# Performance work log

Measured on AMD Instinct MI355X. Metric: run time of the kernel, lower is better.

The kernel has to match this reference:

```python
import jax, jax.numpy as jnp
import numpy as np

B, S, HID = 2, 2048, 2048
H, KV, D = 16, 8, 128          # heads, kv heads, head_dim
GROUPS = H // KV               # 2
RATIO = 0.5
SCALING = D ** -0.5
MIN = float(np.finfo(np.float32).min)


def rotate_half(x):
    x1, x2 = x[..., : D // 2], x[..., D // 2 :]
    return jnp.concatenate((-x2, x1), axis=-1)


def setup_inputs() -> dict:
    key = jax.random.key(0)
    ks = jax.random.split(key, 9)
    hidden_states = jax.random.normal(ks[0], (B, S, HID), jnp.float32)
    # rotary tables (bounded like real cos/sin)
    cos = jax.random.uniform(ks[1], (B, S, D), jnp.float32)
    sin = jax.random.uniform(ks[2], (B, S, D), jnp.float32)
    # additive causal mask [B,1,S,S]: 0 where allowed, finfo.min above diagonal
    causal = jnp.triu(jnp.ones((S, S), bool), k=1)
    attention_mask = jnp.where(causal, MIN, 0.0).astype(jnp.float32)[None, None]
    attention_mask = jnp.broadcast_to(attention_mask, (B, 1, S, S))
    sd = 1.0 / np.sqrt(HID)
    Wq = jax.random.normal(ks[3], (H * D, HID), jnp.float32) * sd
    Wk = jax.random.normal(ks[4], (KV * D, HID), jnp.float32) * sd
    Wv = jax.random.normal(ks[5], (KV * D, HID), jnp.float32) * sd
    A = jax.random.normal(ks[6], (H,), jnp.float32) * 0.1
    Wdt = jax.random.normal(ks[7], (H, KV * D), jnp.float32) * (1.0 / np.sqrt(KV * D))
    Wo = jax.random.normal(ks[8], (HID, H * D), jnp.float32) * (1.0 / np.sqrt(H * D))
    return {"hidden_states": hidden_states, "cos": cos, "sin": sin,
            "attention_mask": attention_mask, "Wq": Wq, "Wk": Wk, "Wv": Wv,
            "A": A, "Wdt": Wdt, "Wo": Wo}


def reference(hidden_states, cos, sin, attention_mask, Wq, Wk, Wv, A, Wdt, Wo):
    x = hidden_states
    # fused QKV projections -> [B, heads, S, D]
    q = (x @ Wq.T).reshape(B, S, H, D).transpose(0, 2, 1, 3)
    k = (x @ Wk.T).reshape(B, S, KV, D).transpose(0, 2, 1, 3)
    v = (x @ Wv.T).reshape(B, S, KV, D).transpose(0, 2, 1, 3)
    # RoPE (cos/sin unsqueezed on head dim)
    c, s = cos[:, None], sin[:, None]
    q = q * c + rotate_half(q) * s
    k = k * c + rotate_half(k) * s
    # dynamic mask: dt_proj(value) -> softplus -> exp, per head  [B, H, S]
    v_flat = v.transpose(0, 2, 1, 3).reshape(B, S, KV * D)
    dt = v_flat @ Wdt.T                                    # [B,S,H]
    dyn = jnp.exp(A * jax.nn.softplus(dt)).transpose(0, 2, 1)  # [B,H,S]
    # kthvalue thresholding (k-th smallest along keys)
    num_dyn = int(S * RATIO)                               # 1024
    kth = jnp.sort(dyn, axis=-1)[..., num_dyn - 1 : num_dyn]   # [B,H,1]
    attn_mask = jnp.where(dyn < kth, MIN, dyn)[:, :, None, :]  # [B,H,1,S]
    attn_mask = attn_mask + attention_mask                 # [B,H,S,S]
    # GQA repeat kv
    k_rep = jnp.repeat(k, GROUPS, axis=1)
    v_rep = jnp.repeat(v, GROUPS, axis=1)
    scores = jnp.einsum("bhqd,bhkd->bhqk", q, k_rep) * SCALING + attn_mask
    w = jax.nn.softmax(scores.astype(jnp.float32), axis=-1).astype(q.dtype)
    out = jnp.einsum("bhqk,bhkd->bhqd", w, v_rep)
    out = out.transpose(0, 2, 1, 3).reshape(B, S, H * D)
    return out @ Wo.T
```

## Files before the change

### kernel.cpp

```cpp
#include <hip/hip_runtime.h>

typedef unsigned short u16;
typedef _Float16 f16x8 __attribute__((ext_vector_type(8)));
typedef float f32x4 __attribute__((ext_vector_type(4)));
typedef u16 u16x8 __attribute__((ext_vector_type(8)));

#define MINF (-0x1.fffffep+127f)
#define SCALE 0.08838834764831845f

__device__ __forceinline__ u16 f2h(float f) {
    _Float16 h = (_Float16)f;
    return __builtin_bit_cast(u16, h);
}
__device__ __forceinline__ float h2f(u16 u) {
    _Float16 h = __builtin_bit_cast(_Float16, u);
    return (float)h;
}

typedef const __attribute__((address_space(1))) void* gptr_t;
typedef __attribute__((address_space(3))) void* sptr_t;
#define GLDS16(g, l) __builtin_amdgcn_global_load_lds((gptr_t)(const void*)(g), (sptr_t)(void*)(l), 16, 0, 0)

__global__ void convk8(const float* __restrict__ in, u16* __restrict__ out, int n) {
    int i = (blockIdx.x * 256 + threadIdx.x) * 8;
    if (i >= n) return;
    f32x4 a = *(const f32x4*)&in[i];
    f32x4 b = *(const f32x4*)&in[i + 4];
    u16x8 r;
#pragma unroll
    for (int j = 0; j < 4; ++j) { r[j] = f2h(a[j]); r[j + 4] = f2h(b[j]); }
    *(u16x8*)&out[i] = r;
}

__global__ void convw3(const float* __restrict__ Wq, const float* __restrict__ Wk,
                       const float* __restrict__ Wv, u16* __restrict__ out) {
    int i = (blockIdx.x * 256 + threadIdx.x) * 8;
    const float* src;
    int off;
    if (i < 4194304) { src = Wq; off = i; }
    else if (i < 6291456) { src = Wk; off = i - 4194304; }
    else { src = Wv; off = i - 6291456; }
    f32x4 a = *(const f32x4*)&src[off];
    f32x4 b = *(const f32x4*)&src[off + 4];
    u16x8 r;
#pragma unroll
    for (int j = 0; j < 4; ++j) { r[j] = f2h(a[j]); r[j + 4] = f2h(b[j]); }
    *(u16x8*)&out[i] = r;
}

__global__ __launch_bounds__(512, 1) void gemm8_qkv(
    const u16* __restrict__ A, const u16* __restrict__ Bw,
    u16* __restrict__ qo, u16* __restrict__ ko, u16* __restrict__ vto) {
    __shared__ alignas(16) u16 AS[2][2][128 * 64];
    __shared__ alignas(16) u16 BS[2][2][128 * 64];
    const int K = 2048, NT = 32;
    int tid = threadIdx.x;
    int wid = tid >> 6, lane = tid & 63;
    int l16 = lane & 15, lhi = lane >> 4;
    int wm = wid >> 2, wn = wid & 3;
    int bm = blockIdx.y * 256, bn = blockIdx.x * 256;
    int srow = lane >> 3;
    int schunk = (lane & 7) ^ srow;
    f32x4 acc[8][4] = {};

    auto STAGE = [&](int t, int buf) {
        int kt = t * 64;
#pragma unroll
        for (int i = 0; i < 2; ++i) {
            int c = wid * 2 + i;
            int row = c * 8 + srow;
            const u16* sa0 = A + (size_t)(bm + row) * K + kt + schunk * 8;
            GLDS16(sa0, &AS[buf][0][c * 512]);
            const u16* sa1 = A + (size_t)(bm + 128 + row) * K + kt + schunk * 8;
            GLDS16(sa1, &AS[buf][1][c * 512]);
            const u16* sb0 = Bw + (size_t)(bn + row) * K + kt + schunk * 8;
            GLDS16(sb0, &BS[buf][0][c * 512]);
            const u16* sb1 = Bw + (size_t)(bn + 128 + row) * K + kt + schunk * 8;
            GLDS16(sb1, &BS[buf][1][c * 512]);
        }
    };

    auto COMPUTE = [&](int buf) {
#pragma unroll
        for (int kk = 0; kk < 2; ++kk) {
            f16x8 af[8], bf[4];
#pragma unroll
            for (int ni = 0; ni < 4; ++ni) {
                int rb = wn * 64 + ni * 16 + l16;
                int half = rb >> 7, rh = rb & 127;
                int c2 = (kk * 4 + lhi) ^ (rh & 7);
                bf[ni] = *(const f16x8*)&BS[buf][half][rh * 64 + c2 * 8];
            }
#pragma unroll
            for (int mi = 0; mi < 8; ++mi) {
                int rh = mi * 16 + l16;
                int c2 = (kk * 4 + lhi) ^ (rh & 7);
                af[mi] = *(const f16x8*)&AS[buf][wm][rh * 64 + c2 * 8];
            }
            __builtin_amdgcn_s_setprio(1);
#pragma unroll
            for (int mi = 0; mi < 8; ++mi)
#pragma unroll
                for (int ni = 0; ni < 4; ++ni)
                    acc[mi][ni] = __builtin_amdgcn_mfma_f32_16x16x32_f16(af[mi], bf[ni], acc[mi][ni], 0, 0, 0);
            __builtin_amdgcn_s_setprio(0);
        }
    };

    STAGE(0, 0);
    STAGE(1, 1);
    asm volatile("s_waitcnt vmcnt(8)" ::: "memory");
    __builtin_amdgcn_sched_barrier(0);
    __builtin_amdgcn_s_barrier();

    for (int t = 0; t < NT; ++t) {
        int buf = t & 1;
        COMPUTE(buf);
        __builtin_amdgcn_s_barrier();
        if (t + 2 < NT) {
            STAGE(t + 2, buf);
            asm volatile("s_waitcnt vmcnt(8)" ::: "memory");
        } else {
            asm volatile("s_waitcnt vmcnt(0)" ::: "memory");
        }
        __builtin_amdgcn_sched_barrier(0);
        __builtin_amdgcn_s_barrier();
    }

#pragma unroll
    for (int mi = 0; mi < 8; ++mi) {
#pragma unroll
        for (int ni = 0; ni < 4; ++ni) {
#pragma unroll
            for (int j = 0; j < 4; ++j) {
                int r = bm + wm * 128 + mi * 16 + lhi * 4 + j;
                int c = bn + wn * 64 + ni * 16 + l16;
                u16 hv = f2h(acc[mi][ni][j]);
                int b = r >> 11, s = r & 2047;
                if (c < 2048) {
                    int hh = c >> 7, d = c & 127;
                    qo[(((size_t)(b * 16 + hh)) * 2048 + s) * 128 + d] = hv;
                } else if (c < 3072) {
                    int hh = (c - 2048) >> 7, d = c & 127;
                    ko[(((size_t)(b * 8 + hh)) * 2048 + s) * 128 + d] = hv;
                } else {
                    int hh = (c - 3072) >> 7, d = c & 127;
                    vto[(((size_t)(b * 8 + hh)) * 128 + d) * 2048 + s] = hv;
                }
            }
        }
    }
}

__global__ __launch_bounds__(512, 1) void gemm8_op(
    const u16* __restrict__ A, const u16* __restrict__ Bw, float* __restrict__ Cf) {
    __shared__ alignas(16) u16 AS[2][2][128 * 64];
    __shared__ alignas(16) u16 BS[2][128 * 64];
    const int K = 2048, NT = 32;
    int tid = threadIdx.x;
    int wid = tid >> 6, lane = tid & 63;
    int l16 = lane & 15, lhi = lane >> 4;
    int wm = wid >> 2, wn = wid & 3;
    int bm = blockIdx.y * 256, bn = blockIdx.x * 128;
    int srow = lane >> 3;
    int schunk = (lane & 7) ^ srow;
    f32x4 acc[8][2] = {};

    auto STAGE = [&](int t, int buf) {
        int kt = t * 64;
#pragma unroll
        for (int i = 0; i < 2; ++i) {
            int c = wid * 2 + i;
            int row = c * 8 + srow;
            const u16* sa0 = A + (size_t)(bm + row) * K + kt + schunk * 8;
            GLDS16(sa0, &AS[buf][0][c * 512]);
            const u16* sa1 = A + (size_t)(bm + 128 + row) * K + kt + schunk * 8;
            GLDS16(sa1, &AS[buf][1][c * 512]);
            const u16* sb0 = Bw + (size_t)(bn + row) * K + kt + schunk * 8;
            GLDS16(sb0, &BS[buf][c * 512]);
        }
    };

    auto COMPUTE = [&](int buf) {
#pragma unroll
        for (int kk = 0; kk < 2; ++kk) {
            f16x8 af[8], bf[2];
#pragma unroll
            for (int ni = 0; ni < 2; ++ni) {
                int rb = wn * 32 + ni * 16 + l16;
                int c2 = (kk * 4 + lhi) ^ (rb & 7);
                bf[ni] = *(const f16x8*)&BS[buf][rb * 64 + c2 * 8];
            }
#pragma unroll
            for (int mi = 0; mi < 8; ++mi) {
                int rh = mi * 16 + l16;
                int c2 = (kk * 4 + lhi) ^ (rh & 7);
                af[mi] = *(const f16x8*)&AS[buf][wm][rh * 64 + c2 * 8];
            }
            __builtin_amdgcn_s_setprio(1);
#pragma unroll
            for (int mi = 0; mi < 8; ++mi)
#pragma unroll
                for (int ni = 0; ni < 2; ++ni)
                    acc[mi][ni] = __builtin_amdgcn_mfma_f32_16x16x32_f16(af[mi], bf[ni], acc[mi][ni], 0, 0, 0);
            __builtin_amdgcn_s_setprio(0);
        }
    };

    STAGE(0, 0);
    STAGE(1, 1);
    asm volatile("s_waitcnt vmcnt(6)" ::: "memory");
    __builtin_amdgcn_sched_barrier(0);
    __builtin_amdgcn_s_barrier();

    for (int t = 0; t < NT; ++t) {
        int buf = t & 1;
        COMPUTE(buf);
        __builtin_amdgcn_s_barrier();
        if (t + 2 < NT) {
            STAGE(t + 2, buf);
            asm volatile("s_waitcnt vmcnt(6)" ::: "memory");
        } else {
            asm volatile("s_waitcnt vmcnt(0)" ::: "memory");
        }
        __builtin_amdgcn_sched_barrier(0);
        __builtin_amdgcn_s_barrier();
    }

#pragma unroll
    for (int mi = 0; mi < 8; ++mi)
#pragma unroll
        for (int ni = 0; ni < 2; ++ni)
#pragma unroll
            for (int j = 0; j < 4; ++j) {
                int r = bm + wm * 128 + mi * 16 + lhi * 4 + j;
                int c = bn + wn * 32 + ni * 16 + l16;
                Cf[(size_t)r * 2048 + c] = acc[mi][ni][j];
            }
}

__global__ void rope_fused(u16* __restrict__ q, u16* __restrict__ k,
                           const float* __restrict__ cosv, const float* __restrict__ sinv) {
    int i = blockIdx.x * 256 + threadIdx.x;
    int d = i & 63;
    int s = (i >> 6) & 2047;
    int b = i >> 17;
    size_t cb = ((size_t)b * 2048 + s) * 128;
    float c1 = cosv[cb + d], s1 = sinv[cb + d];
    float c2 = cosv[cb + d + 64], s2 = sinv[cb + d + 64];
#pragma unroll
    for (int h = 0; h < 16; ++h) {
        size_t base = (((size_t)(b * 16 + h)) * 2048 + s) * 128;
        float x1 = h2f(q[base + d]), x2 = h2f(q[base + d + 64]);
        q[base + d] = f2h(x1 * c1 - x2 * s1);
        q[base + d + 64] = f2h(x2 * c2 + x1 * s2);
    }
#pragma unroll
    for (int h = 0; h < 8; ++h) {
        size_t base = (((size_t)(b * 8 + h)) * 2048 + s) * 128;
        float x1 = h2f(k[base + d]), x2 = h2f(k[base + d + 64]);
        k[base + d] = f2h(x1 * c1 - x2 * s1);
        k[base + d + 64] = f2h(x2 * c2 + x1 * s2);
    }
}

__global__ void wdtv_kernel(const float* __restrict__ Wdt, const float* __restrict__ Wv,
                            float* __restrict__ out) {
    int t = threadIdx.x;
    int h = blockIdx.x >> 3;
    int c = (blockIdx.x & 7) * 256 + t;
    const float* wd = Wdt + h * 1024;
    float acc = 0.f;
    for (int f = 0; f < 1024; ++f) acc += wd[f] * Wv[(size_t)f * 2048 + c];
    out[h * 2048 + c] = acc;
}

__global__ void dt_dyn_kernel(const float* __restrict__ x, const float* __restrict__ Wdtv,
                              const float* __restrict__ Av, float* __restrict__ dyn) {
    __shared__ float xrow[2048];
    __shared__ float red[256];
    int bs = blockIdx.x;
    int t = threadIdx.x;
    for (int i = t; i < 2048; i += 256) xrow[i] = x[(size_t)bs * 2048 + i];
    __syncthreads();
    int h = t & 15, chunk = t >> 4;
    float p = 0.f;
    const float* wrow = Wdtv + h * 2048 + chunk * 128;
    const float* xr = xrow + chunk * 128;
    for (int f = 0; f < 128; ++f) p += xr[f] * wrow[f];
    red[t] = p;
    __syncthreads();
    if (t < 16) {
        float dt = 0.f;
        for (int c = 0; c < 16; ++c) dt += red[c * 16 + t];
        float sp = fmaxf(dt, 0.f) + log1pf(expf(-fabsf(dt)));
        int b = bs >> 11, s = bs & 2047;
        dyn[((size_t)(b * 16 + t)) * 2048 + s] = expf(Av[t] * sp);
    }
}

__global__ void kth_mask_kernel(const float* __restrict__ dyn, float* __restrict__ mval) {
    __shared__ float sv[2048];
    int bh = blockIdx.x, t = threadIdx.x;
    const float* row = dyn + (size_t)bh * 2048;
    sv[t] = row[t];
    sv[t + 1024] = row[t + 1024];
    __syncthreads();
    for (int k = 2; k <= 2048; k <<= 1) {
        for (int j = k >> 1; j > 0; j >>= 1) {
#pragma unroll 1
            for (int base = 0; base < 2048; base += 1024) {
                int i = base + t;
                int ixj = i ^ j;
                if (ixj > i) {
                    float a = sv[i], b = sv[ixj];
                    bool up = ((i & k) == 0);
                    if ((a > b) == up) { sv[i] = b; sv[ixj] = a; }
                }
            }
            __syncthreads();
        }
    }
    float kth = sv[1023];
    float v0 = row[t];
    float v1 = row[t + 1024];
    mval[(size_t)bh * 2048 + t] = v0 < kth ? MINF : v0;
    mval[(size_t)bh * 2048 + t + 1024] = v1 < kth ? MINF : v1;
}

__global__ __launch_bounds__(256) void attn_kernel(
    const u16* __restrict__ qb, const u16* __restrict__ kb, const u16* __restrict__ vtb,
    const float* __restrict__ mv, u16* __restrict__ ao) {
    __shared__ alignas(16) u16 Kst[2][64 * 128];
    __shared__ alignas(16) u16 Vst[2][128 * 64];
    __shared__ alignas(16) u16 plds[4][16 * 72];
    __shared__ int flags[4];
    int bh = blockIdx.x;
    int qt = 31 - blockIdx.y;
    int b = bh >> 4, h = bh & 15, kvh = h >> 1;
    int wid = threadIdx.x >> 6, lane = threadIdx.x & 63;
    int l16 = lane & 15, lhi = lane >> 4;
    int q0 = qt * 64 + wid * 16;
    const u16* qbase = qb + (((size_t)bh * 2048) + q0) * 128;
    const u16* kbase = kb + ((size_t)(b * 8 + kvh) * 2048) * 128;
    const u16* vtbase = vtb + ((size_t)(b * 8 + kvh) * 128) * 2048;
    const float* mvb = mv + (size_t)bh * 2048;
    u16* pw = plds[wid];
    int rx = l16 & 7;

    auto STAGE = [&](int kt2, int bidx) {
        int kvb2 = kt2 * 64;
#pragma unroll
        for (int i = 0; i < 4; ++i) {
            int call = wid * 4 + i;
            int r = call * 4 + (lane >> 4);
            int gch = (lane & 15) ^ (r & 7);
            const u16* src = kbase + (size_t)(kvb2 + r) * 128 + gch * 8;
            GLDS16(src, &Kst[bidx][call * 512]);
        }
#pragma unroll
        for (int i = 0; i < 4; ++i) {
            int call = wid * 4 + i;
            int d = call * 8 + (lane >> 3);
            int gch = (lane & 7) ^ (d & 7);
            const u16* src = vtbase + (size_t)d * 2048 + kvb2 + gch * 8;
            GLDS16(src, &Vst[bidx][call * 512]);
        }
    };

    f16x8 qf[4];
#pragma unroll
    for (int kc = 0; kc < 4; ++kc) qf[kc] = *(const f16x8*)&qbase[l16 * 128 + kc * 32 + lhi * 8];
    f16x8 ones;
#pragma unroll
    for (int i = 0; i < 8; ++i) ones[i] = (_Float16)1.f;
    float m[4];
#pragma unroll
    for (int j = 0; j < 4; ++j) m[j] = -INFINITY;
    f32x4 accO[8] = {};
    f32x4 accS = {};

    STAGE(0, 0);
    __syncthreads();

    for (int kt = 0; kt < 32; ++kt) {
        if (kt > qt) {
            if (!(flags[0] | flags[1] | flags[2] | flags[3])) break;
        }
        int buf = kt & 1;
        if (kt + 1 < 32) STAGE(kt + 1, buf ^ 1);
        int kvb = kt * 64;

        f32x4 sc[4] = {};
#pragma unroll
        for (int ni = 0; ni < 4; ++ni) {
            const u16* kr = &Kst[buf][(ni * 16 + l16) * 128];
#pragma unroll
            for (int kc = 0; kc < 4; ++kc) {
                int cc = (kc * 4 + lhi) ^ rx;
                f16x8 kf = *(const f16x8*)&kr[cc * 8];
                sc[ni] = __builtin_amdgcn_mfma_f32_16x16x32_f16(qf[kc], kf, sc[ni], 0, 0, 0);
            }
        }

        float rmax[4] = {-INFINITY, -INFINITY, -INFINITY, -INFINITY};
#pragma unroll
        for (int ni = 0; ni < 4; ++ni) {
            int key = kvb + ni * 16 + l16;
            float mk = mvb[key];
#pragma unroll
            for (int j = 0; j < 4; ++j) {
                int qrow = q0 + lhi * 4 + j;
                float sval = sc[ni][j] * SCALE + (mk + (key > qrow ? MINF : 0.f));
                sc[ni][j] = sval;
                rmax[j] = fmaxf(rmax[j], sval);
            }
        }
#pragma unroll
        for (int j = 0; j < 4; ++j) {
#pragma unroll
            for (int off = 1; off < 16; off <<= 1) rmax[j] = fmaxf(rmax[j], __shfl_xor(rmax[j], off));
        }
        float mn[4];
        bool need = false;
#pragma unroll
        for (int j = 0; j < 4; ++j) {
            mn[j] = fmaxf(m[j], rmax[j]);
            need |= (mn[j] - m[j] > 8.0f);
        }
        if (__any(need)) {
#pragma unroll
            for (int j = 0; j < 4; ++j) {
                float r = __expf(m[j] - mn[j]);
                m[j] = mn[j];
                accS[j] *= r;
#pragma unroll
                for (int db = 0; db < 8; ++db) accO[db][j] *= r;
            }
        }
#pragma unroll
        for (int ni = 0; ni < 4; ++ni) {
#pragma unroll
            for (int j = 0; j < 4; ++j) {
                float pv = __expf(sc[ni][j] - m[j]);
                pw[(lhi * 4 + j) * 72 + ni * 16 + l16] = f2h(pv);
            }
        }

#pragma unroll
        for (int kc2 = 0; kc2 < 2; ++kc2) {
            f16x8 pa = *(const f16x8*)&pw[l16 * 72 + kc2 * 32 + lhi * 8];
            accS = __builtin_amdgcn_mfma_f32_16x16x32_f16(pa, ones, accS, 0, 0, 0);
#pragma unroll
            for (int db = 0; db < 8; ++db) {
                int cc = (kc2 * 4 + lhi) ^ rx;
                f16x8 vf = *(const f16x8*)&Vst[buf][(db * 16 + l16) * 64 + cc * 8];
                accO[db] = __builtin_amdgcn_mfma_f32_16x16x32_f16(pa, vf, accO[db], 0, 0, 0);
            }
        }

        bool deg = (m[0] == MINF) | (m[1] == MINF) | (m[2] == MINF) | (m[3] == MINF);
        if (lane == 0) flags[wid] = __any(deg) ? 1 : 0;
        __syncthreads();
    }

#pragma unroll
    for (int db = 0; db < 8; ++db) {
#pragma unroll
        for (int j = 0; j < 4; ++j) {
            int qrow = q0 + lhi * 4 + j;
            int d = db * 16 + l16;
            float o = accO[db][j] / accS[j];
            ao[((size_t)(b * 2048) + qrow) * 2048 + h * 128 + d] = f2h(o);
        }
    }
}

extern "C" void kernel_launch(void* const* d_in, const int* in_sizes, int n_in,
                              void* d_out, int out_size, void* d_ws, size_t ws_size,
                              hipStream_t stream) {
    const float* x = (const float*)d_in[0];
    const float* cosv = (const float*)d_in[1];
    const float* sinv = (const float*)d_in[2];
    const float* Wq = (const float*)d_in[4];
    const float* Wk = (const float*)d_in[5];
    const float* Wv = (const float*)d_in[6];
    const float* Av = (const float*)d_in[7];
    const float* Wdt = (const float*)d_in[8];
    const float* Wo = (const float*)d_in[9];

    char* ws = (char*)d_ws;
    u16* qb = (u16*)(ws);
    u16* kb = (u16*)(ws + 16777216);
    u16* vtb = (u16*)(ws + 25165824);
    float* dyn = (float*)(ws + 33554432);
    float* mval = (float*)(ws + 33816576);
    float* wdtv = (float*)(ws + 34078720);
    u16* xbf = (u16*)(ws + 34209792);
    u16* wbf = (u16*)(ws + 50987008);

    convk8<<<8388608 / 2048, 256, 0, stream>>>(x, xbf, 8388608);
    convw3<<<8388608 / 2048, 256, 0, stream>>>(Wq, Wk, Wv, wbf);

    dim3 g1(16, 16);
    gemm8_qkv<<<g1, 512, 0, stream>>>(xbf, wbf, qb, kb, vtb);

    rope_fused<<<1024, 256, 0, stream>>>(qb, kb, cosv, sinv);

    wdtv_kernel<<<128, 256, 0, stream>>>(Wdt, Wv, wdtv);
    dt_dyn_kernel<<<4096, 256, 0, stream>>>(x, wdtv, Av, dyn);
    kth_mask_kernel<<<32, 1024, 0, stream>>>(dyn, mval);

    convk8<<<4194304 / 2048, 256, 0, stream>>>(Wo, wbf, 4194304);

    dim3 g2(32, 32);
    attn_kernel<<<g2, 256, 0, stream>>>(qb, kb, vtb, mval, xbf);

    dim3 g3(16, 16);
    gemm8_op<<<g3, 512, 0, stream>>>(xbf, wbf, (float*)d_out);
}
```

Measured before the change: 443.3 us.

## Replace bitonic sort with radix-select to find kth dynamic-mask threshold

The kth-smallest search over each 2048-element row now uses a four-pass 8-bit radix select on the float bit patterns, with a shared-memory histogram and a serial prefix scan. This replaces the full bitonic sort, which needed 66 barrier-separated passes. Blocks shrink from 1024 to 256 threads. The bit-pattern ordering only holds because the dyn values are positive (exp outputs), and the serial 256-bin scan on one thread adds some latency per pass.

```diff
diff --git a/kernel.cpp b/kernel.cpp
--- a/kernel.cpp
+++ b/kernel.cpp
@@ -300,32 +300,45 @@
 }
 
 __global__ void kth_mask_kernel(const float* __restrict__ dyn, float* __restrict__ mval) {
-    __shared__ float sv[2048];
+    __shared__ unsigned int sv[2048];
+    __shared__ unsigned int hist[256];
+    __shared__ unsigned int ctrl[2];
     int bh = blockIdx.x, t = threadIdx.x;
-    const float* row = dyn + (size_t)bh * 2048;
-    sv[t] = row[t];
-    sv[t + 1024] = row[t + 1024];
+    const unsigned int* row = (const unsigned int*)(dyn + (size_t)bh * 2048);
+#pragma unroll
+    for (int i = 0; i < 8; ++i) sv[t + i * 256] = row[t + i * 256];
+    if (t == 0) { ctrl[0] = 0u; ctrl[1] = 1024u; }
+#pragma unroll
+    for (int shift = 24; shift >= 0; shift -= 8) {
+        __syncthreads();
+        hist[t] = 0u;
+        __syncthreads();
+        unsigned int prefix = ctrl[0];
+        unsigned int hmask = (shift == 24) ? 0u : (0xFFFFFFFFu << (shift + 8));
+#pragma unroll
+        for (int i = 0; i < 8; ++i) {
+            unsigned int u = sv[t + i * 256];
+            if ((u & hmask) == prefix) atomicAdd(&hist[(u >> shift) & 255], 1u);
+        }
+        __syncthreads();
+        if (t == 0) {
+            unsigned int r = ctrl[1], cum = 0u;
+            for (int bb = 0; bb < 256; ++bb) {
+                unsigned int c = hist[bb];
+                if (cum + c >= r) { ctrl[0] = prefix | ((unsigned int)bb << shift); ctrl[1] = r - cum; break; }
+                cum += c;
+            }
+        }
+    }
     __syncthreads();
-    for (int k = 2; k <= 2048; k <<= 1) {
-        for (int j = k >> 1; j > 0; j >>= 1) {
-#pragma unroll 1
-            for (int base = 0; base < 2048; base += 1024) {
-                int i = base + t;
-                int ixj = i ^ j;
-                if (ixj > i) {
-                    float a = sv[i], b = sv[ixj];
-                    bool up = ((i & k) == 0);
-                    if ((a > b) == up) { sv[i] = b; sv[ixj] = a; }
-                }
-            }
-            __syncthreads();
-        }
-    }
-    float kth = sv[1023];
-    float v0 = row[t];
-    float v1 = row[t + 1024];
-    mval[(size_t)bh * 2048 + t] = v0 < kth ? MINF : v0;
-    mval[(size_t)bh * 2048 + t + 1024] = v1 < kth ? MINF : v1;
+    float kth = __uint_as_float(ctrl[0]);
+    float* mrow = mval + (size_t)bh * 2048;
+#pragma unroll
+    for (int i = 0; i < 8; ++i) {
+        int idx = t + i * 256;
+        float v = __uint_as_float(sv[idx]);
+        mrow[idx] = v < kth ? MINF : v;
+    }
 }
 
 __global__ __launch_bounds__(256) void attn_kernel(
@@ -509,7 +522,7 @@
 
     wdtv_kernel<<<128, 256, 0, stream>>>(Wdt, Wv, wdtv);
     dt_dyn_kernel<<<4096, 256, 0, stream>>>(x, wdtv, Av, dyn);
-    kth_mask_kernel<<<32, 1024, 0, stream>>>(dyn, mval);
+    kth_mask_kernel<<<32, 256, 0, stream>>>(dyn, mval);
 
     convk8<<<4194304 / 2048, 256, 0, stream>>>(Wo, wbf, 4194304);
 
```

New measurement: 464.2 us. 1.05x slower.
